# Kernel optimization log

Measured on AMD Instinct MI355X. Metric: run time of the kernel, lower is better.

Reference implementation:

```python
import jax, jax.numpy as jnp
import numpy as np


def setup_inputs() -> dict:
    key = jax.random.key(0)
    k1, k2, k3 = jax.random.split(key, 3)
    x = jax.random.normal(k1, (16, 64, 256, 256), dtype=jnp.float32)
    conv_weight = jax.random.normal(k2, (128, 64, 3, 3), dtype=jnp.float32) * 0.05
    conv_bias = jax.random.normal(k3, (128,), dtype=jnp.float32) * 0.05
    return {"x": x, "conv_weight": conv_weight, "conv_bias": conv_bias}


def reference(x, conv_weight, conv_bias):
    # Conv2d: stride 1, padding 0, dilation 1, groups 1 -> [B, out_c, 254, 254]
    y = jax.lax.conv_general_dilated(
        x, conv_weight,
        window_strides=(1, 1),
        padding="VALID",
        dimension_numbers=("NCHW", "OIHW", "NCHW"),
    ) + conv_bias[None, :, None, None]
    # Min over output channels (keepdim), then double tanh -> [B, 1, 254, 254]
    m = jnp.min(y, axis=1, keepdims=True)
    return jnp.tanh(jnp.tanh(m))
```

## Files before the change

kernel.cpp:

```cpp
#include <hip/hip_runtime.h>
#include <math.h>


typedef __attribute__((ext_vector_type(8))) short bf16x8;
typedef __attribute__((ext_vector_type(16))) float f32x16;

static __device__ __forceinline__ short f2bf(float f) {
    unsigned u = __float_as_uint(f);
    u += 0x7fffu + ((u >> 16) & 1u);
    return (short)(u >> 16);
}

__global__ void wtrans(const float* __restrict__ wg, short* __restrict__ wsB) {
    int o4 = blockIdx.x * 256 + threadIdx.x;
    if (o4 >= 18432) return;
    float4 v = ((const float4*)wg)[o4];
    float f[4] = {v.x, v.y, v.z, v.w};
    int base = o4 * 4;
    #pragma unroll
    for (int q = 0; q < 4; ++q) {
        int e  = base + q;
        int kw = e % 3, r1 = e / 3;
        int kh = r1 % 3, r2 = r1 / 3;
        int ic = r2 & 63, oc = r2 >> 6;
        int tap = kh * 3 + kw;
        int icc = ic >> 4, hi = (ic >> 3) & 1, j = ic & 7;
        int kstep = tap * 4 + icc;
        wsB[((kstep * 2 + hi) * 128 + oc) * 8 + j] = f2bf(f[q]);
    }
}

__global__ __launch_bounds__(256, 3)
void conv_min_tanh_mfma(const float* __restrict__ xg,
                        const short* __restrict__ wsB,
                        const float* __restrict__ bg,
                        float* __restrict__ out) {
    __shared__ __align__(16) short xt[16896];

    const int tid  = threadIdx.x;
    const int lane = tid & 63, l31 = lane & 31, hi = lane >> 5;
    const int w    = tid >> 6;
    const int r    = w & 1;
    const int nh   = w >> 1;
    const int ow0  = blockIdx.x * 64;
    const int oh0  = blockIdx.y * 2;
    const int b    = blockIdx.z;

    #pragma unroll
    for (int t = 0; t < 9; ++t) {
        int idx = t * 256 + tid;
        if (idx < 2112) {
            int g   = idx / 66;
            int col = idx - g * 66;
            int row = g >> 3;
            int icb = ((g >> 1) & 3) * 16 + (g & 1) * 8;
            int iw  = ow0 + col;
            const float* src = xg + (((size_t)(b * 64 + icb) * 256) + (oh0 + row)) * 256 + iw;
            bool valid = iw < 256;
            float f[8];
            #pragma unroll
            for (int j = 0; j < 8; ++j) f[j] = valid ? src[j * 65536] : 0.f;
            bf16x8 v;
            #pragma unroll
            for (int j = 0; j < 8; ++j) v[j] = f2bf(f[j]);
            *(bf16x8*)(xt + g * 528 + col * 8) = v;
        }
    }

    const bf16x8* bbase = (const bf16x8*)(wsB + ((size_t)hi * 128 + nh * 64 + l31) * 8);

    bf16x8 bc0 = bbase[0],   bc1 = bbase[32];
    bf16x8 bd0 = bbase[256], bd1 = bbase[256 + 32];
    bf16x8 be0 = bd0, be1 = bd1;

    __syncthreads();

    f32x16 acc00 = {}, acc01 = {}, acc10 = {}, acc11 = {};

    const bf16x8* ap0 = (const bf16x8*)(xt + ((r * 4 + 0) * 2 + hi) * 528 + l31 * 8);
    bf16x8 a0 = ap0[0], a1 = ap0[32];

    #pragma unroll
    for (int k = 0; k < 36; ++k) {
        if (k < 34) {
            be0 = bbase[(k + 2) * 256];
            be1 = bbase[(k + 2) * 256 + 32];
        }
        bf16x8 an0 = a0, an1 = a1;
        if (k < 35) {
            const int kn = k + 1, tapn = kn >> 2, iccn = kn & 3;
            const int khn = tapn / 3, kwn = tapn - khn * 3;
            const bf16x8* apn = (const bf16x8*)(xt +
                (((r + khn) * 4 + iccn) * 2 + hi) * 528 + (l31 + kwn) * 8);
            an0 = apn[0];
            an1 = apn[32];
        }
        acc00 = __builtin_amdgcn_mfma_f32_32x32x16_bf16(a0, bc0, acc00, 0, 0, 0);
        acc01 = __builtin_amdgcn_mfma_f32_32x32x16_bf16(a0, bc1, acc01, 0, 0, 0);
        acc10 = __builtin_amdgcn_mfma_f32_32x32x16_bf16(a1, bc0, acc10, 0, 0, 0);
        acc11 = __builtin_amdgcn_mfma_f32_32x32x16_bf16(a1, bc1, acc11, 0, 0, 0);
        a0 = an0; a1 = an1;
        bc0 = bd0; bc1 = bd1;
        bd0 = be0; bd1 = be1;
    }

    __syncthreads();
    float* sm = (float*)xt;
    const float bv0 = bg[nh * 64 + l31];
    const float bv1 = bg[nh * 64 + 32 + l31];
    #pragma unroll
    for (int reg = 0; reg < 16; ++reg) {
        const int m = (reg & 3) + 8 * (reg >> 2) + 4 * hi;
        float p0 = fminf(acc00[reg] + bv0, acc01[reg] + bv1);
        float p1 = fminf(acc10[reg] + bv0, acc11[reg] + bv1);
        sm[(r * 64 + m) * 65 + nh * 32 + l31]      = p0;
        sm[(r * 64 + 32 + m) * 65 + nh * 32 + l31] = p1;
    }
    __syncthreads();
    {
        const int px = tid >> 1, half = tid & 1;
        const float* rowp = sm + px * 65 + half * 32;
        float v = rowp[0];
        #pragma unroll
        for (int j = 1; j < 32; ++j) v = fminf(v, rowp[j]);
        v = fminf(v, __shfl_xor(v, 1, 64));
        if (half == 0) {
            v = tanhf(tanhf(v));
            const int ow = ow0 + (px & 63);
            const int oh = oh0 + (px >> 6);
            if (ow < 254)
                out[((size_t)b * 254 + oh) * 254 + ow] = v;
        }
    }
}

extern "C" void kernel_launch(void* const* d_in, const int* in_sizes, int n_in,
                              void* d_out, int out_size, void* d_ws, size_t ws_size,
                              hipStream_t stream) {
    const float* x  = (const float*)d_in[0];
    const float* wg = (const float*)d_in[1];
    const float* bs = (const float*)d_in[2];
    float* out = (float*)d_out;
    short* wsB = (short*)d_ws;

    wtrans<<<72, 256, 0, stream>>>(wg, wsB);
    dim3 grid(4, 127, 16);
    conv_min_tanh_mfma<<<grid, 256, 0, stream>>>(x, wsB, bs, out);
}
```

Baseline: 489.7 us.

## Pipeline input staging by channel chunk and reorder K loop per chunk

Splits the global-to-LDS staging of the input tile into four 16-channel chunks held in two register buffers, so loading later chunks overlaps MFMA work on earlier ones. The K loop is reordered to go chunk-major (channel chunk outer, tap inner), with weight prefetch indices rewritten to follow that order. The float-to-bf16 conversion now uses the packed v_cvt_pk_bf16_f32 instruction. In exchange it adds three extra barriers and about 48 more registers for the staging buffers, which may cut occupancy under the 3-blocks launch bound.

```diff
diff --git a/kernel.cpp b/kernel.cpp
--- a/kernel.cpp
+++ b/kernel.cpp
@@ -9,6 +9,12 @@
     unsigned u = __float_as_uint(f);
     u += 0x7fffu + ((u >> 16) & 1u);
     return (short)(u >> 16);
+}
+
+static __device__ __forceinline__ unsigned cvt_pk_bf16(float a, float b) {
+    unsigned r;
+    asm("v_cvt_pk_bf16_f32 %0, %1, %2" : "=v"(r) : "v"(a), "v"(b));
+    return r;
 }
 
 __global__ void wtrans(const float* __restrict__ wg, short* __restrict__ wsB) {
@@ -30,6 +36,39 @@
     }
 }
 
+#define STAGE_ISSUE(c, f)                                                     \
+    _Pragma("unroll")                                                         \
+    for (int s = 0; s < 3; ++s) {                                             \
+        int v = s * 256 + tid;                                                \
+        if (v < 528) {                                                        \
+            int gl = v / 66, col = v - gl * 66;                               \
+            int row = gl >> 1, hie = gl & 1;                                  \
+            int iw = ow0 + col;                                               \
+            const float* src = xg +                                           \
+                (((size_t)(b * 64 + (c) * 16 + hie * 8) * 256) +              \
+                 (oh0 + row)) * 256 + iw;                                     \
+            bool valid = iw < 256;                                            \
+            _Pragma("unroll")                                                 \
+            for (int j = 0; j < 8; ++j) f[s][j] = valid ? src[j * 65536] : 0.f; \
+        }                                                                     \
+    }
+
+#define STAGE_WRITE(c, f)                                                     \
+    _Pragma("unroll")                                                         \
+    for (int s = 0; s < 3; ++s) {                                             \
+        int v = s * 256 + tid;                                                \
+        if (v < 528) {                                                        \
+            int gl = v / 66, col = v - gl * 66;                               \
+            int row = gl >> 1, hie = gl & 1;                                  \
+            bf16x8 vv;                                                        \
+            unsigned* vp = (unsigned*)&vv;                                    \
+            _Pragma("unroll")                                                 \
+            for (int p = 0; p < 4; ++p)                                       \
+                vp[p] = cvt_pk_bf16(f[s][2 * p], f[s][2 * p + 1]);            \
+            *(bf16x8*)(xt + (row * 8 + (c) * 2 + hie) * 528 + col * 8) = vv;  \
+        }                                                                     \
+    }
+
 __global__ __launch_bounds__(256, 3)
 void conv_min_tanh_mfma(const float* __restrict__ xg,
                         const short* __restrict__ wsB,
@@ -46,62 +85,58 @@
     const int oh0  = blockIdx.y * 2;
     const int b    = blockIdx.z;
 
-    #pragma unroll
-    for (int t = 0; t < 9; ++t) {
-        int idx = t * 256 + tid;
-        if (idx < 2112) {
-            int g   = idx / 66;
-            int col = idx - g * 66;
-            int row = g >> 3;
-            int icb = ((g >> 1) & 3) * 16 + (g & 1) * 8;
-            int iw  = ow0 + col;
-            const float* src = xg + (((size_t)(b * 64 + icb) * 256) + (oh0 + row)) * 256 + iw;
-            bool valid = iw < 256;
-            float f[8];
-            #pragma unroll
-            for (int j = 0; j < 8; ++j) f[j] = valid ? src[j * 65536] : 0.f;
-            bf16x8 v;
-            #pragma unroll
-            for (int j = 0; j < 8; ++j) v[j] = f2bf(f[j]);
-            *(bf16x8*)(xt + g * 528 + col * 8) = v;
-        }
-    }
+    const bf16x8* bbase = (const bf16x8*)(wsB + ((size_t)hi * 128 + nh * 64 + l31) * 8);
+    bf16x8 bc0 = bbase[0],       bc1 = bbase[32];
+    bf16x8 bd0 = bbase[4 * 256], bd1 = bbase[4 * 256 + 32];
 
-    const bf16x8* bbase = (const bf16x8*)(wsB + ((size_t)hi * 128 + nh * 64 + l31) * 8);
-
-    bf16x8 bc0 = bbase[0],   bc1 = bbase[32];
-    bf16x8 bd0 = bbase[256], bd1 = bbase[256 + 32];
-    bf16x8 be0 = bd0, be1 = bd1;
-
+    float fA[3][8], fB[3][8];
+    STAGE_ISSUE(0, fA)
+    STAGE_ISSUE(1, fB)
+    STAGE_WRITE(0, fA)
     __syncthreads();
 
     f32x16 acc00 = {}, acc01 = {}, acc10 = {}, acc11 = {};
 
-    const bf16x8* ap0 = (const bf16x8*)(xt + ((r * 4 + 0) * 2 + hi) * 528 + l31 * 8);
-    bf16x8 a0 = ap0[0], a1 = ap0[32];
+    #pragma unroll
+    for (int icc = 0; icc < 4; ++icc) {
+        if (icc == 0) { STAGE_ISSUE(2, fA) }
+        if (icc == 1) { STAGE_ISSUE(3, fB) }
 
-    #pragma unroll
-    for (int k = 0; k < 36; ++k) {
-        if (k < 34) {
-            be0 = bbase[(k + 2) * 256];
-            be1 = bbase[(k + 2) * 256 + 32];
+        const bf16x8* ap = (const bf16x8*)(xt + ((r * 4 + icc) * 2 + hi) * 528 + l31 * 8);
+        bf16x8 a0 = ap[0], a1 = ap[32];
+
+        #pragma unroll
+        for (int t = 0; t < 9; ++t) {
+            bf16x8 an0 = a0, an1 = a1;
+            if (t < 8) {
+                const int tapn = t + 1, khn = tapn / 3, kwn = tapn - khn * 3;
+                const bf16x8* apn = (const bf16x8*)(xt +
+                    (((r + khn) * 4 + icc) * 2 + hi) * 528 + (l31 + kwn) * 8);
+                an0 = apn[0];
+                an1 = apn[32];
+            }
+            bf16x8 be0 = bd0, be1 = bd1;
+            if (t < 7) {
+                const int kp = (t + 2) * 4 + icc;
+                be0 = bbase[kp * 256];
+                be1 = bbase[kp * 256 + 32];
+            } else if (icc < 3) {
+                const int kp = (t - 7) * 4 + icc + 1;
+                be0 = bbase[kp * 256];
+                be1 = bbase[kp * 256 + 32];
+            }
+            acc00 = __builtin_amdgcn_mfma_f32_32x32x16_bf16(a0, bc0, acc00, 0, 0, 0);
+            acc01 = __builtin_amdgcn_mfma_f32_32x32x16_bf16(a0, bc1, acc01, 0, 0, 0);
+            acc10 = __builtin_amdgcn_mfma_f32_32x32x16_bf16(a1, bc0, acc10, 0, 0, 0);
+            acc11 = __builtin_amdgcn_mfma_f32_32x32x16_bf16(a1, bc1, acc11, 0, 0, 0);
+            a0 = an0; a1 = an1;
+            bc0 = bd0; bc1 = bd1;
+            bd0 = be0; bd1 = be1;
         }
-        bf16x8 an0 = a0, an1 = a1;
-        if (k < 35) {
-            const int kn = k + 1, tapn = kn >> 2, iccn = kn & 3;
-            const int khn = tapn / 3, kwn = tapn - khn * 3;
-            const bf16x8* apn = (const bf16x8*)(xt +
-                (((r + khn) * 4 + iccn) * 2 + hi) * 528 + (l31 + kwn) * 8);
-            an0 = apn[0];
-            an1 = apn[32];
-        }
-        acc00 = __builtin_amdgcn_mfma_f32_32x32x16_bf16(a0, bc0, acc00, 0, 0, 0);
-        acc01 = __builtin_amdgcn_mfma_f32_32x32x16_bf16(a0, bc1, acc01, 0, 0, 0);
-        acc10 = __builtin_amdgcn_mfma_f32_32x32x16_bf16(a1, bc0, acc10, 0, 0, 0);
-        acc11 = __builtin_amdgcn_mfma_f32_32x32x16_bf16(a1, bc1, acc11, 0, 0, 0);
-        a0 = an0; a1 = an1;
-        bc0 = bd0; bc1 = bd1;
-        bd0 = be0; bd1 = be1;
+
+        if (icc == 0) { STAGE_WRITE(1, fB) __syncthreads(); }
+        if (icc == 1) { STAGE_WRITE(2, fA) __syncthreads(); }
+        if (icc == 2) { STAGE_WRITE(3, fB) __syncthreads(); }
     }
 
     __syncthreads();
```

Result: faster. 472.6 us (-3.5%).

## Stream input rows through a rotating LDS ring across multiple output row pairs per block

Applied to the files above, without the earlier changes.

Each block now handles up to 11 output row pairs instead of one. It keeps a 6-row circular buffer of bf16-converted input in LDS and prefetches the next two rows into registers while the MFMA loop runs, so each input row is loaded roughly once per block instead of twice. The channel-min reduction now uses in-register shuffles plus a small obuf instead of a padded LDS transpose, and conversion uses the packed v_cvt_pk_bf16 instruction. The grid shrinks to 768 blocks with more LDS per block, which reduces parallelism and may lower occupancy or leave the GPU's CUs unevenly loaded.

```diff
diff --git a/kernel.cpp b/kernel.cpp
--- a/kernel.cpp
+++ b/kernel.cpp
@@ -9,6 +9,12 @@
     unsigned u = __float_as_uint(f);
     u += 0x7fffu + ((u >> 16) & 1u);
     return (short)(u >> 16);
+}
+
+static __device__ __forceinline__ unsigned cvt_pk_bf16(float a, float b) {
+    unsigned r;
+    asm("v_cvt_pk_bf16_f32 %0, %1, %2" : "=v"(r) : "v"(a), "v"(b));
+    return r;
 }
 
 __global__ void wtrans(const float* __restrict__ wg, short* __restrict__ wsB) {
@@ -30,12 +36,45 @@
     }
 }
 
+#define STAGE1_ISSUE(rg, fbuf)                                                \
+    _Pragma("unroll")                                                         \
+    for (int s = 0; s < 3; ++s) {                                             \
+        int idx = s * 256 + tid;                                              \
+        if (idx < 528) {                                                      \
+            int g = idx / 66, col = idx - g * 66;                             \
+            int icc = g >> 1, hie = g & 1;                                    \
+            int iw = ow0 + col;                                               \
+            const float* src = xg +                                           \
+                (((size_t)(b * 64 + icc * 16 + hie * 8) * 256) + (rg)) * 256 + iw; \
+            bool valid = iw < 256;                                            \
+            _Pragma("unroll")                                                 \
+            for (int j = 0; j < 8; ++j) fbuf[s][j] = valid ? src[j * 65536] : 0.f; \
+        }                                                                     \
+    }
+
+#define STAGE1_WRITE(ss, fbuf)                                                \
+    _Pragma("unroll")                                                         \
+    for (int s = 0; s < 3; ++s) {                                             \
+        int idx = s * 256 + tid;                                              \
+        if (idx < 528) {                                                      \
+            int g = idx / 66, col = idx - g * 66;                             \
+            int icc = g >> 1, hie = g & 1;                                    \
+            bf16x8 vv;                                                        \
+            unsigned* vp = (unsigned*)&vv;                                    \
+            _Pragma("unroll")                                                 \
+            for (int p = 0; p < 4; ++p)                                       \
+                vp[p] = cvt_pk_bf16(fbuf[s][2 * p], fbuf[s][2 * p + 1]);      \
+            *(bf16x8*)(xt + ((ss) * 8 + icc * 2 + hie) * 528 + col * 8) = vv; \
+        }                                                                     \
+    }
+
 __global__ __launch_bounds__(256, 3)
 void conv_min_tanh_mfma(const float* __restrict__ xg,
                         const short* __restrict__ wsB,
                         const float* __restrict__ bg,
                         float* __restrict__ out) {
-    __shared__ __align__(16) short xt[16896];
+    __shared__ __align__(16) short xt[25344];
+    __shared__ float obuf[256];
 
     const int tid  = threadIdx.x;
     const int lane = tid & 63, l31 = lane & 31, hi = lane >> 5;
@@ -43,94 +82,122 @@
     const int r    = w & 1;
     const int nh   = w >> 1;
     const int ow0  = blockIdx.x * 64;
-    const int oh0  = blockIdx.y * 2;
     const int b    = blockIdx.z;
-
-    #pragma unroll
-    for (int t = 0; t < 9; ++t) {
-        int idx = t * 256 + tid;
-        if (idx < 2112) {
-            int g   = idx / 66;
-            int col = idx - g * 66;
-            int row = g >> 3;
-            int icb = ((g >> 1) & 3) * 16 + (g & 1) * 8;
-            int iw  = ow0 + col;
-            const float* src = xg + (((size_t)(b * 64 + icb) * 256) + (oh0 + row)) * 256 + iw;
-            bool valid = iw < 256;
-            float f[8];
-            #pragma unroll
-            for (int j = 0; j < 8; ++j) f[j] = valid ? src[j * 65536] : 0.f;
-            bf16x8 v;
-            #pragma unroll
-            for (int j = 0; j < 8; ++j) v[j] = f2bf(f[j]);
-            *(bf16x8*)(xt + g * 528 + col * 8) = v;
-        }
-    }
+    const int p0   = blockIdx.y * 11;
+    const int np   = min(11, 127 - p0);
+    const int ih0  = p0 * 2;
 
     const bf16x8* bbase = (const bf16x8*)(wsB + ((size_t)hi * 128 + nh * 64 + l31) * 8);
-
     bf16x8 bc0 = bbase[0],   bc1 = bbase[32];
     bf16x8 bd0 = bbase[256], bd1 = bbase[256 + 32];
-    bf16x8 be0 = bd0, be1 = bd1;
-
-    __syncthreads();
-
-    f32x16 acc00 = {}, acc01 = {}, acc10 = {}, acc11 = {};
-
-    const bf16x8* ap0 = (const bf16x8*)(xt + ((r * 4 + 0) * 2 + hi) * 528 + l31 * 8);
-    bf16x8 a0 = ap0[0], a1 = ap0[32];
-
-    #pragma unroll
-    for (int k = 0; k < 36; ++k) {
-        if (k < 34) {
-            be0 = bbase[(k + 2) * 256];
-            be1 = bbase[(k + 2) * 256 + 32];
-        }
-        bf16x8 an0 = a0, an1 = a1;
-        if (k < 35) {
-            const int kn = k + 1, tapn = kn >> 2, iccn = kn & 3;
-            const int khn = tapn / 3, kwn = tapn - khn * 3;
-            const bf16x8* apn = (const bf16x8*)(xt +
-                (((r + khn) * 4 + iccn) * 2 + hi) * 528 + (l31 + kwn) * 8);
-            an0 = apn[0];
-            an1 = apn[32];
-        }
-        acc00 = __builtin_amdgcn_mfma_f32_32x32x16_bf16(a0, bc0, acc00, 0, 0, 0);
-        acc01 = __builtin_amdgcn_mfma_f32_32x32x16_bf16(a0, bc1, acc01, 0, 0, 0);
-        acc10 = __builtin_amdgcn_mfma_f32_32x32x16_bf16(a1, bc0, acc10, 0, 0, 0);
-        acc11 = __builtin_amdgcn_mfma_f32_32x32x16_bf16(a1, bc1, acc11, 0, 0, 0);
-        a0 = an0; a1 = an1;
-        bc0 = bd0; bc1 = bd1;
-        bd0 = be0; bd1 = be1;
-    }
-
-    __syncthreads();
-    float* sm = (float*)xt;
+
+    {
+        float fP[3][8], fQ[3][8];
+        STAGE1_ISSUE(ih0 + 0, fP)
+        STAGE1_ISSUE(ih0 + 1, fQ)
+        STAGE1_WRITE(0, fP)
+        STAGE1_WRITE(1, fQ)
+        STAGE1_ISSUE(ih0 + 2, fP)
+        STAGE1_ISSUE(ih0 + 3, fQ)
+        STAGE1_WRITE(2, fP)
+        STAGE1_WRITE(3, fQ)
+    }
     const float bv0 = bg[nh * 64 + l31];
     const float bv1 = bg[nh * 64 + 32 + l31];
-    #pragma unroll
-    for (int reg = 0; reg < 16; ++reg) {
-        const int m = (reg & 3) + 8 * (reg >> 2) + 4 * hi;
-        float p0 = fminf(acc00[reg] + bv0, acc01[reg] + bv1);
-        float p1 = fminf(acc10[reg] + bv0, acc11[reg] + bv1);
-        sm[(r * 64 + m) * 65 + nh * 32 + l31]      = p0;
-        sm[(r * 64 + 32 + m) * 65 + nh * 32 + l31] = p1;
-    }
     __syncthreads();
-    {
-        const int px = tid >> 1, half = tid & 1;
-        const float* rowp = sm + px * 65 + half * 32;
-        float v = rowp[0];
+
+    int s0 = r, s1 = r + 1, s2 = r + 2;
+    int sA = 4, sB = 5;
+    float fS[3][8];
+
+    for (int it = 0; it < np; ++it) {
+        const bool do_stage = (it < np - 1);
+        if (do_stage) { STAGE1_ISSUE(ih0 + 2 * it + 4, fS) }
+
+        const bf16x8* bp0 = (const bf16x8*)(xt + (s0 * 8 + hi) * 528 + l31 * 8);
+        const bf16x8* bp1 = (const bf16x8*)(xt + (s1 * 8 + hi) * 528 + l31 * 8);
+        const bf16x8* bp2 = (const bf16x8*)(xt + (s2 * 8 + hi) * 528 + l31 * 8);
+
+        f32x16 acc00 = {}, acc01 = {}, acc10 = {}, acc11 = {};
+        bf16x8 a0 = bp0[0], a1 = bp0[32];
+
         #pragma unroll
-        for (int j = 1; j < 32; ++j) v = fminf(v, rowp[j]);
-        v = fminf(v, __shfl_xor(v, 1, 64));
-        if (half == 0) {
-            v = tanhf(tanhf(v));
-            const int ow = ow0 + (px & 63);
-            const int oh = oh0 + (px >> 6);
-            if (ow < 254)
-                out[((size_t)b * 254 + oh) * 254 + ow] = v;
-        }
+        for (int k = 0; k < 36; ++k) {
+            if (k == 18) {
+                if (do_stage) {
+                    STAGE1_WRITE(sA, fS)
+                    STAGE1_ISSUE(ih0 + 2 * it + 5, fS)
+                }
+            }
+            bf16x8 an0 = a0, an1 = a1;
+            if (k < 35) {
+                const int kn = k + 1, tapn = kn >> 2, iccn = kn & 3;
+                const int khn = tapn / 3, kwn = tapn - khn * 3;
+                const bf16x8* bp = (khn == 0) ? bp0 : (khn == 1) ? bp1 : bp2;
+                an0 = bp[iccn * 132 + kwn];
+                an1 = bp[iccn * 132 + kwn + 32];
+            }
+            bf16x8 be0 = bd0, be1 = bd1;
+            if (k < 34) {
+                be0 = bbase[(k + 2) * 256];
+                be1 = bbase[(k + 2) * 256 + 32];
+            }
+            acc00 = __builtin_amdgcn_mfma_f32_32x32x16_bf16(a0, bc0, acc00, 0, 0, 0);
+            acc01 = __builtin_amdgcn_mfma_f32_32x32x16_bf16(a0, bc1, acc01, 0, 0, 0);
+            acc10 = __builtin_amdgcn_mfma_f32_32x32x16_bf16(a1, bc0, acc10, 0, 0, 0);
+            acc11 = __builtin_amdgcn_mfma_f32_32x32x16_bf16(a1, bc1, acc11, 0, 0, 0);
+            a0 = an0; a1 = an1;
+            bc0 = bd0; bc1 = bd1;
+            bd0 = be0; bd1 = be1;
+        }
+
+        if (do_stage) { STAGE1_WRITE(sB, fS) }
+        bc0 = bbase[0];   bc1 = bbase[32];
+        bd0 = bbase[256]; bd1 = bbase[256 + 32];
+
+        __syncthreads();
+
+        float v[32];
+        #pragma unroll
+        for (int reg = 0; reg < 16; ++reg) {
+            v[reg]      = fminf(acc00[reg] + bv0, acc01[reg] + bv1);
+            v[16 + reg] = fminf(acc10[reg] + bv0, acc11[reg] + bv1);
+        }
+        #pragma unroll
+        for (int mbit = 1; mbit <= 16; mbit <<= 1) {
+            const int cnt = 16 / mbit;
+            bool up = (l31 & mbit) != 0;
+            #pragma unroll
+            for (int j = 0; j < cnt; ++j) {
+                float send = up ? v[j] : v[j + cnt];
+                float recv = __shfl_xor(send, mbit, 64);
+                float mine = up ? v[j + cnt] : v[j];
+                v[j] = fminf(mine, recv);
+            }
+        }
+        {
+            int ridx = ((l31 & 1) << 4) | ((l31 & 2) << 2) | (l31 & 4) |
+                       ((l31 & 8) >> 2) | ((l31 & 16) >> 4);
+            int mm = ridx & 15;
+            int px = ((ridx >> 4) << 5) + (mm & 3) + ((mm >> 2) << 3) + (hi << 2);
+            obuf[nh * 128 + r * 64 + px] = v[0];
+        }
+        __syncthreads();
+
+        if (tid < 128) {
+            float x = fminf(obuf[tid], obuf[128 + tid]);
+            x = tanhf(tanhf(x));
+            const int col = tid & 63, row = tid >> 6;
+            const int oh = (p0 + it) * 2 + row;
+            if (ow0 + col < 254)
+                out[((size_t)b * 254 + oh) * 254 + ow0 + col] = x;
+        }
+
+        s0 += 2; if (s0 >= 6) s0 -= 6;
+        s1 += 2; if (s1 >= 6) s1 -= 6;
+        s2 += 2; if (s2 >= 6) s2 -= 6;
+        sA += 2; if (sA >= 6) sA -= 6;
+        sB += 2; if (sB >= 6) sB -= 6;
     }
 }
 
@@ -144,6 +211,6 @@
     short* wsB = (short*)d_ws;
 
     wtrans<<<72, 256, 0, stream>>>(wg, wsB);
-    dim3 grid(4, 127, 16);
+    dim3 grid(4, 12, 16);
     conv_min_tanh_mfma<<<grid, 256, 0, stream>>>(x, wsB, bs, out);
 }
```

Result: slower. 944.4 us (+92.9%).
